# Kernel tuning notes

Hardware: AMD Instinct MI355X
Metric: run time of the kernel (lower is better)

## Reference

```python
import jax, jax.numpy as jnp
import numpy as np

B, S, E, H = 2, 2048, 1024, 16
HD = E // H  # head dim = 64
BASE = 10000.0


def _rope(x):
    # x: [b, h, s, hd]; interleaved RoPE (pairs (2i, 2i+1) rotated)
    s, hd = x.shape[-2], x.shape[-1]
    theta = 1.0 / (BASE ** (jnp.arange(0, hd, 2, dtype=jnp.float32) / hd))  # [hd/2]
    enc = jnp.arange(s, dtype=jnp.float32)[:, None] * theta[None, :]        # [s, hd/2]
    enc = jnp.repeat(enc, 2, axis=-1)                                        # [s, hd] interleaved
    cos, sin = jnp.cos(enc), jnp.sin(enc)
    # rotate_half: (x1, x2) -> (-x2, x1) on interleaved pairs
    xp = x.reshape(*x.shape[:-1], hd // 2, 2)
    rot = jnp.stack((-xp[..., 1], xp[..., 0]), axis=-1).reshape(x.shape)
    return x * cos + rot * sin


def reference(x, w1, w2):
    b, s, e = x.shape
    qkv = jnp.einsum('bse,fe->bsf', x, w1)                 # [b, s, 3e]
    qkv = qkv.reshape(b, s, 3, H, HD)                      # 'b s (n h e)'
    q, k, v = (jnp.transpose(qkv[:, :, i], (0, 2, 1, 3)) for i in range(3))  # [b,h,s,hd]
    q, k = _rope(q), _rope(k)
    scale = 1.0 / jnp.sqrt(jnp.asarray(HD, dtype=x.dtype))
    scores = jnp.einsum('bhqd,bhkd->bhqk', q, k) * scale   # [b,h,s,s]
    attn = jax.nn.softmax(scores, axis=-1)
    o = jnp.einsum('bhqk,bhkd->bhqd', attn, v)             # [b,h,s,hd]
    o = jnp.transpose(o, (0, 2, 1, 3)).reshape(b, s, e)    # 'b h s e -> b s (h e)'
    return jnp.einsum('bse,fe->bsf', o, w2)


def setup_inputs() -> dict:
    key = jax.random.key(0)
    k1, k2, k3 = jax.random.split(key, 3)
    x = jax.random.normal(k1, (B, S, E), dtype=jnp.float32)
    w1 = jax.random.normal(k2, (3 * E, E), dtype=jnp.float32) * (E ** -0.5)
    w2 = jax.random.normal(k3, (E, E), dtype=jnp.float32) * (E ** -0.5)
    return {"x": x, "w1": w1, "w2": w2}
```

## Files before the change

kernel.cpp:

```cpp
#include <hip/hip_runtime.h>
#include <math.h>

typedef unsigned short u16;
typedef unsigned int u32;
typedef float f32x4 __attribute__((ext_vector_type(4)));
typedef float f32x16 __attribute__((ext_vector_type(16)));
typedef u32 u32x4 __attribute__((ext_vector_type(4)));

static const size_t TAB_B  = 0;
static const size_t QBF_B  = 524288;
static const size_t KBF_B  = 8912896;
static const size_t VTB_B  = 17301504;
static const size_t W2H_B  = 25690112;
static const size_t XBF_B  = 29884416;
static const size_t W1BF_B = 38273024;
static const size_t O16_B  = 29884416;

#if __has_builtin(__builtin_amdgcn_exp2f)
#define EXP2(x) __builtin_amdgcn_exp2f(x)
#else
#define EXP2(x) __expf(0.69314718056f * (x))
#endif

__device__ __forceinline__ u16 f2bf(float f) {
  u32 u = __builtin_bit_cast(u32, f);
  u += 0x7fffu + ((u >> 16) & 1u);
  return (u16)(u >> 16);
}
__device__ __forceinline__ float bf2f(u16 h) {
  return __builtin_bit_cast(float, (u32)h << 16);
}
__device__ __forceinline__ u16 f2h(float f) {
  _Float16 h = (_Float16)f;
  return __builtin_bit_cast(u16, h);
}
__device__ __forceinline__ u32 cvtpk(float a, float b) {
  u32 r;
  asm("v_cvt_pk_bf16_f32 %0, %1, %2" : "=v"(r) : "v"(a), "v"(b));
  return r;
}
__device__ __forceinline__ void plswap(u32& a, u32& b) {
  asm volatile("v_permlane32_swap_b32 %0, %1" : "+v"(a), "+v"(b));
}
__device__ __forceinline__ void mfma16(f32x4& d, u32x4 a, u32x4 b) {
  asm volatile("v_mfma_f32_16x16x32_bf16 %0, %1, %2, %0"
               : "+v"(d)
               : "v"(a), "v"(b));
}
__device__ __forceinline__ void mfma16f(f32x4& d, u32x4 a, u32x4 b) {
  asm volatile("v_mfma_f32_16x16x32_f16 %0, %1, %2, %0"
               : "+v"(d)
               : "v"(a), "v"(b));
}
__device__ __forceinline__ void mfma32(f32x16& d, u32x4 a, u32x4 b) {
  asm volatile("v_mfma_f32_32x32x16_bf16 %0, %1, %2, %0"
               : "+v"(d)
               : "v"(a), "v"(b));
}
__device__ __forceinline__ void gld16(const void* g, void* l) {
  __builtin_amdgcn_global_load_lds(
      (const __attribute__((address_space(1))) void*)(void*)g,
      (__attribute__((address_space(3))) void*)l, 16, 0, 0);
}
#define HZ()                                            \
  do {                                                  \
    asm volatile("s_nop 7\ns_nop 7\ns_nop 7\ns_nop 7"); \
    __builtin_amdgcn_sched_barrier(0);                  \
  } while (0)

__global__ __launch_bounds__(256) void prep_kernel(
    const float* __restrict__ x, const float* __restrict__ w1,
    const float* __restrict__ w2, float2* __restrict__ tab,
    u16* __restrict__ xbf, u16* __restrict__ w1bf, u16* __restrict__ w2h) {
  const int blk = blockIdx.x;
  const int t = threadIdx.x;
  if (blk < 256) {
    const int idx = (blk << 8) + t;
    const int s = idx >> 5, i = idx & 31;
    double theta = pow(10000.0, -((double)(2 * i)) / 64.0);
    float ang = (float)s * (float)theta;
    tab[idx] = make_float2(cosf(ang), sinf(ang));
  } else if (blk < 1280) {
    int i = ((blk - 256) << 8) + t;
#pragma unroll
    for (int r = 0; r < 4; ++r, i += 262144) {
      float4 v = ((const float4*)x)[i];
      ushort4 o;
      o.x = f2bf(v.x); o.y = f2bf(v.y); o.z = f2bf(v.z); o.w = f2bf(v.w);
      ((ushort4*)xbf)[i] = o;
    }
  } else if (blk < 2048) {
    int i = ((blk - 1280) << 8) + t;
#pragma unroll
    for (int r = 0; r < 4; ++r, i += 196608) {
      float4 v = ((const float4*)w1)[i];
      ushort4 o;
      o.x = f2bf(v.x); o.y = f2bf(v.y); o.z = f2bf(v.z); o.w = f2bf(v.w);
      ((ushort4*)w1bf)[i] = o;
    }
  } else {
    int i = ((blk - 2048) << 8) + t;
#pragma unroll
    for (int r = 0; r < 4; ++r, i += 65536) {
      float4 v = ((const float4*)w2)[i];
      ushort4 o;
      o.x = f2h(v.x); o.y = f2h(v.y); o.z = f2h(v.z); o.w = f2h(v.w);
      ((ushort4*)w2h)[i] = o;
    }
  }
}

template <int MODE>
__global__ __launch_bounds__(256) void gemm_bt(
    const u16* __restrict__ Ahi, const u16* __restrict__ Bhi, int nbn, int nkb,
    const float2* __restrict__ tab, u16* __restrict__ qd, u16* __restrict__ kd,
    u16* __restrict__ vtd, float* __restrict__ fout) {
  __shared__ __align__(16) char As[16384];
  __shared__ __align__(16) char Bs[16384];
  const int bm = blockIdx.x / nbn;
  const int bn = blockIdx.x % nbn;
  const int m0 = bm << 7;
  const int n0 = bn << 7;
  const int t = threadIdx.x;
  const int w = t >> 6;
  const int lane = t & 63;
  const int lr = lane & 15;
  const int lg = lane >> 4;
  const int wr0 = (w >> 1) << 6;
  const int wc0 = (w & 1) << 6;
  const int srow0 = t >> 3;
  const int sblk = t & 7;

  f32x4 acc[4][4];
#pragma unroll
  for (int mi = 0; mi < 4; ++mi)
#pragma unroll
    for (int ni = 0; ni < 4; ++ni) acc[mi][ni] = (f32x4)0.0f;

  for (int kb = 0; kb < nkb; ++kb) {
    const int k0 = kb << 6;
    if (kb) __syncthreads();
#pragma unroll
    for (int r = 0; r < 4; ++r) {
      const int row = srow0 + (r << 5);
      const int g = sblk ^ (row & 7);
      gld16(Ahi + (size_t)(m0 + row) * 1024 + k0 + (g << 3),
            As + (r << 12) + (w << 10));
      gld16(Bhi + (size_t)(n0 + row) * 1024 + k0 + (g << 3),
            Bs + (r << 12) + (w << 10));
    }
    asm volatile("s_waitcnt vmcnt(0)" ::: "memory");
    __syncthreads();
#pragma unroll
    for (int kk = 0; kk < 2; ++kk) {
      u32x4 af[4], bf[4];
#pragma unroll
      for (int mi = 0; mi < 4; ++mi) {
        const int row = wr0 + (mi << 4) + lr;
        af[mi] = *(const u32x4*)(As + row * 128 +
                                 ((((kk << 2) + lg) ^ (row & 7)) << 4));
      }
#pragma unroll
      for (int ni = 0; ni < 4; ++ni) {
        const int row = wc0 + (ni << 4) + lr;
        bf[ni] = *(const u32x4*)(Bs + row * 128 +
                                 ((((kk << 2) + lg) ^ (row & 7)) << 4));
      }
      asm volatile("s_nop 1");
      __builtin_amdgcn_s_setprio(1);
#pragma unroll
      for (int mi = 0; mi < 4; ++mi)
#pragma unroll
        for (int ni = 0; ni < 4; ++ni) {
          if constexpr (MODE == 1)
            mfma16f(acc[mi][ni], af[mi], bf[ni]);
          else
            mfma16(acc[mi][ni], af[mi], bf[ni]);
        }
      __builtin_amdgcn_s_setprio(0);
    }
  }
  HZ();
#pragma unroll
  for (int mi = 0; mi < 4; ++mi)
#pragma unroll
    for (int ni = 0; ni < 4; ++ni)
#pragma unroll
      for (int i = 0; i < 4; ++i) {
        float val = acc[mi][ni][i];
        const int grow = m0 + wr0 + (mi << 4) + (lg << 2) + i;
        const int col = n0 + wc0 + (ni << 4) + lr;
        if (MODE == 0) {
          const int b = grow >> 11, s = grow & 2047;
          const int which = col >> 10, hh = (col >> 6) & 15, d = col & 63;
          const size_t base = (size_t)((b << 4) + hh);
          if (which == 2) {
            vtd[(base * 64 + d) * 2048 + s] = f2bf(val);
          } else {
            float other = __shfl_xor(val, 1);
            float2 cs = tab[(s << 5) + (d >> 1)];
            float r = (d & 1) ? fmaf(val, cs.x, other * cs.y)
                              : fmaf(val, cs.x, -other * cs.y);
            if (which == 0) r *= 0.18033688011f;
            u16* dst = which ? kd : qd;
            dst[(base * 2048 + s) * 64 + d] = f2bf(r);
          }
        } else {
          fout[(size_t)grow * 1024 + col] = val;
        }
      }
}

__global__ __launch_bounds__(256) void attn_mfma(
    const u16* __restrict__ q, const u16* __restrict__ k,
    const u16* __restrict__ vt, u16* __restrict__ o16) {
  __shared__ __align__(16) char Ks[2][8192];
  __shared__ __align__(16) char Vs[2][8192];
  const int bid = blockIdx.x;
  const int swz = (bid & 7) * 64 + (bid >> 3);
  const int qt = swz & 15;
  const int hh = (swz >> 4) & 15;
  const int b = swz >> 8;
  const int t = threadIdx.x;
  const int w = t >> 6;
  const int lane = t & 63;
  const int lq = lane & 31;
  const int h = lane >> 5;

  const size_t bh = (size_t)((b << 4) + hh);
  const u16* qb = q + (bh * 2048 + (size_t)(qt * 128 + w * 32)) * 64;
  const u16* kb = k + bh * 2048 * 64;
  const u16* vb = vt + bh * 64 * 2048;

  u32x4 qf[4];
#pragma unroll
  for (int dk = 0; dk < 4; ++dk)
    qf[dk] = *(const u32x4*)(qb + lq * 64 + dk * 16 + h * 8);

  auto issue = [&](int kt_, int buf_) {
    const u16* ksrc = kb + kt_ * 4096;
#pragma unroll
    for (int r = 0; r < 2; ++r) {
      const int row = (t >> 3) + (r << 5);
      const int g = (t & 7) ^ (row & 7);
      gld16(ksrc + row * 64 + (g << 3), &Ks[buf_][(r << 12) + (w << 10)]);
      gld16(vb + (size_t)row * 2048 + kt_ * 64 + (g << 3),
            &Vs[buf_][(r << 12) + (w << 10)]);
    }
  };

  f32x16 oacc0 = (f32x16)0.0f, oacc1 = (f32x16)0.0f;
  float lrow = 0.0f;

  issue(0, 0);
  for (int kt = 0; kt < 32; ++kt) {
    const int cur = kt & 1;
    if (kt < 31) {
      issue(kt + 1, cur ^ 1);
      asm volatile("s_waitcnt vmcnt(4)" ::: "memory");
    } else {
      asm volatile("s_waitcnt vmcnt(0)" ::: "memory");
    }
    __syncthreads();
    const char* Kc = Ks[cur];
    const char* Vc = Vs[cur];
    f32x16 s0 = (f32x16)0.0f, s1 = (f32x16)0.0f;
    __builtin_amdgcn_s_setprio(1);
#pragma unroll
    for (int dk = 0; dk < 4; ++dk) {
      const int c = (dk << 1) + h;
      u32x4 kf0 = *(const u32x4*)(Kc + lq * 128 + ((c ^ (lq & 7)) << 4));
      u32x4 kf1 = *(const u32x4*)(Kc + (32 + lq) * 128 + ((c ^ (lq & 7)) << 4));
      mfma32(s0, kf0, qf[dk]);
      mfma32(s1, kf1, qf[dk]);
    }
    __builtin_amdgcn_s_setprio(0);
    HZ();
    float lsum = 0.0f;
#pragma unroll
    for (int i = 0; i < 16; ++i) {
      s0[i] = EXP2(s0[i]);
      lsum += s0[i];
    }
#pragma unroll
    for (int i = 0; i < 16; ++i) {
      s1[i] = EXP2(s1[i]);
      lsum += s1[i];
    }
    lrow += lsum;
    u32x4 pa0, pa1, pa2, pa3;
    {
      u32 w0 = cvtpk(s0[0], s0[1]), w1 = cvtpk(s0[2], s0[3]);
      u32 w2 = cvtpk(s0[4], s0[5]), w3 = cvtpk(s0[6], s0[7]);
      u32 w4 = cvtpk(s0[8], s0[9]), w5 = cvtpk(s0[10], s0[11]);
      u32 w6 = cvtpk(s0[12], s0[13]), w7 = cvtpk(s0[14], s0[15]);
      plswap(w0, w2);
      plswap(w1, w3);
      plswap(w4, w6);
      plswap(w5, w7);
      pa0[0] = w0; pa0[1] = w1; pa0[2] = w2; pa0[3] = w3;
      pa1[0] = w4; pa1[1] = w5; pa1[2] = w6; pa1[3] = w7;
      u32 y0 = cvtpk(s1[0], s1[1]), y1 = cvtpk(s1[2], s1[3]);
      u32 y2 = cvtpk(s1[4], s1[5]), y3 = cvtpk(s1[6], s1[7]);
      u32 y4 = cvtpk(s1[8], s1[9]), y5 = cvtpk(s1[10], s1[11]);
      u32 y6 = cvtpk(s1[12], s1[13]), y7 = cvtpk(s1[14], s1[15]);
      plswap(y0, y2);
      plswap(y1, y3);
      plswap(y4, y6);
      plswap(y5, y7);
      pa2[0] = y0; pa2[1] = y1; pa2[2] = y2; pa2[3] = y3;
      pa3[0] = y4; pa3[1] = y5; pa3[2] = y6; pa3[3] = y7;
    }
    asm volatile("s_nop 2");
    __builtin_amdgcn_s_setprio(1);
#define PVSTEP(kbk, paf)                                                      \
  {                                                                           \
    const int c = ((kbk) << 1) + h;                                           \
    u32x4 vf0 = *(const u32x4*)(Vc + lq * 128 + ((c ^ (lq & 7)) << 4));       \
    u32x4 vf1 =                                                               \
        *(const u32x4*)(Vc + (32 + lq) * 128 + ((c ^ (lq & 7)) << 4));        \
    mfma32(oacc0, paf, vf0);                                                  \
    mfma32(oacc1, paf, vf1);                                                  \
  }
    PVSTEP(0, pa0)
    PVSTEP(1, pa1)
    PVSTEP(2, pa2)
    PVSTEP(3, pa3)
#undef PVSTEP
    __builtin_amdgcn_s_setprio(0);
    __syncthreads();
  }
  HZ();
  const float invl = 1.0f / (lrow + __shfl_xor(lrow, 32));
#pragma unroll
  for (int r = 0; r < 16; ++r) {
    const int qr = (r & 3) + 8 * (r >> 2) + 4 * h;
    const float fr = __shfl(invl, qr);
    const size_t srow = (size_t)(b * 2048 + (qt << 7) + (w << 5) + qr);
    const size_t base = srow * 1024 + (hh << 6) + lq;
    o16[base] = f2h(oacc0[r] * fr);
    o16[base + 32] = f2h(oacc1[r] * fr);
  }
}

extern "C" void kernel_launch(void* const* d_in, const int* in_sizes, int n_in,
                              void* d_out, int out_size, void* d_ws,
                              size_t ws_size, hipStream_t stream) {
  const float* x = (const float*)d_in[0];
  const float* w1 = (const float*)d_in[1];
  const float* w2 = (const float*)d_in[2];
  char* ws = (char*)d_ws;
  float2* tab = (float2*)(ws + TAB_B);
  u16* qbf = (u16*)(ws + QBF_B);
  u16* kbf = (u16*)(ws + KBF_B);
  u16* vtbf = (u16*)(ws + VTB_B);
  u16* w2h = (u16*)(ws + W2H_B);
  u16* xbf = (u16*)(ws + XBF_B);
  u16* w1bf = (u16*)(ws + W1BF_B);
  u16* o16 = (u16*)(ws + O16_B);
  float* out = (float*)d_out;

  prep_kernel<<<dim3(2304), dim3(256), 0, stream>>>(x, w1, w2, tab, xbf, w1bf,
                                                    w2h);
  gemm_bt<0><<<dim3(32 * 24), dim3(256), 0, stream>>>(
      xbf, w1bf, 24, 16, tab, qbf, kbf, vtbf, nullptr);
  attn_mfma<<<dim3(512), dim3(256), 0, stream>>>(qbf, kbf, vtbf, o16);
  gemm_bt<1><<<dim3(32 * 8), dim3(256), 0, stream>>>(
      o16, w2h, 8, 16, nullptr, nullptr, nullptr, nullptr, out);
}
```

Before: 127.4 us.

## Stage V transpose through LDS for coalesced stores and swizzle GEMM blocks across XCDs

In the QKV GEMM, V tiles are written transposed into shared memory and then stored to global memory as contiguous 16-byte rows, replacing scattered 2-byte strided writes. Block ids are also remapped so that neighbouring tiles land on the same XCD, which should improve L2 reuse. This costs extra LDS, two barriers in the V blocks and a slightly larger shared allocation.

```diff
diff --git a/kernel.cpp b/kernel.cpp
--- a/kernel.cpp
+++ b/kernel.cpp
@@ -113,12 +113,15 @@
 template <int MODE>
 __global__ __launch_bounds__(256) void gemm_bt(
     const u16* __restrict__ Ahi, const u16* __restrict__ Bhi, int nbn, int nkb,
-    const float2* __restrict__ tab, u16* __restrict__ qd, u16* __restrict__ kd,
-    u16* __restrict__ vtd, float* __restrict__ fout) {
-  __shared__ __align__(16) char As[16384];
-  __shared__ __align__(16) char Bs[16384];
-  const int bm = blockIdx.x / nbn;
-  const int bn = blockIdx.x % nbn;
+    int cpx, const float2* __restrict__ tab, u16* __restrict__ qd,
+    u16* __restrict__ kd, u16* __restrict__ vtd, float* __restrict__ fout) {
+  __shared__ __align__(16) char SMEM[34816];
+  char* As = SMEM;
+  char* Bs = SMEM + 16384;
+  const int bid = blockIdx.x;
+  const int wgid = (bid & 7) * cpx + (bid >> 3);
+  const int bm = wgid / nbn;
+  const int bn = wgid % nbn;
   const int m0 = bm << 7;
   const int n0 = bn << 7;
   const int t = threadIdx.x;
@@ -181,6 +184,33 @@
     }
   }
   HZ();
+  if (MODE == 0 && n0 >= 2048) {
+    u16* Vt = (u16*)SMEM;
+    __syncthreads();
+#pragma unroll
+    for (int mi = 0; mi < 4; ++mi)
+#pragma unroll
+      for (int ni = 0; ni < 4; ++ni)
+#pragma unroll
+        for (int i = 0; i < 4; ++i) {
+          const int dl = wc0 + (ni << 4) + lr;
+          const int sl = wr0 + (mi << 4) + (lg << 2) + i;
+          Vt[dl * 136 + sl] = f2bf(acc[mi][ni][i]);
+        }
+    __syncthreads();
+    const int row = t >> 1;
+    const int half = t & 1;
+    const int hh2 = (n0 - 2048 + row) >> 6;
+    const int d2 = (n0 - 2048 + row) & 63;
+    const int b2 = m0 >> 11;
+    u16* dst = vtd + (((size_t)(b2 * 16 + hh2) * 64 + d2) * 2048) +
+               (m0 & 2047) + half * 64;
+    const u16* src = Vt + row * 136 + half * 64;
+#pragma unroll
+    for (int c = 0; c < 8; ++c)
+      *(u32x4*)(dst + (c << 3)) = *(const u32x4*)(src + (c << 3));
+    return;
+  }
 #pragma unroll
   for (int mi = 0; mi < 4; ++mi)
 #pragma unroll
@@ -194,17 +224,13 @@
           const int b = grow >> 11, s = grow & 2047;
           const int which = col >> 10, hh = (col >> 6) & 15, d = col & 63;
           const size_t base = (size_t)((b << 4) + hh);
-          if (which == 2) {
-            vtd[(base * 64 + d) * 2048 + s] = f2bf(val);
-          } else {
-            float other = __shfl_xor(val, 1);
-            float2 cs = tab[(s << 5) + (d >> 1)];
-            float r = (d & 1) ? fmaf(val, cs.x, other * cs.y)
-                              : fmaf(val, cs.x, -other * cs.y);
-            if (which == 0) r *= 0.18033688011f;
-            u16* dst = which ? kd : qd;
-            dst[(base * 2048 + s) * 64 + d] = f2bf(r);
-          }
+          float other = __shfl_xor(val, 1);
+          float2 cs = tab[(s << 5) + (d >> 1)];
+          float r = (d & 1) ? fmaf(val, cs.x, other * cs.y)
+                            : fmaf(val, cs.x, -other * cs.y);
+          if (which == 0) r *= 0.18033688011f;
+          u16* dstp = which ? kd : qd;
+          dstp[(base * 2048 + s) * 64 + d] = f2bf(r);
         } else {
           fout[(size_t)grow * 1024 + col] = val;
         }
@@ -363,8 +389,8 @@
   prep_kernel<<<dim3(2304), dim3(256), 0, stream>>>(x, w1, w2, tab, xbf, w1bf,
                                                     w2h);
   gemm_bt<0><<<dim3(32 * 24), dim3(256), 0, stream>>>(
-      xbf, w1bf, 24, 16, tab, qbf, kbf, vtbf, nullptr);
+      xbf, w1bf, 24, 16, 96, tab, qbf, kbf, vtbf, nullptr);
   attn_mfma<<<dim3(512), dim3(256), 0, stream>>>(qbf, kbf, vtbf, o16);
   gemm_bt<1><<<dim3(32 * 8), dim3(256), 0, stream>>>(
-      o16, w2h, 8, 16, nullptr, nullptr, nullptr, nullptr, out);
-}
+      o16, w2h, 8, 16, 32, nullptr, nullptr, nullptr, nullptr, out);
+}
```

Result: faster. 111.1 us (-12.8%).
